# Kernel optimization log

Measured on AMD Instinct MI355X. Metric: run time of the kernel, lower is better.

Reference implementation:

```python
import jax, jax.numpy as jnp
import numpy as np

B, N, E = 64, 2048, 32768
F_IN, NHID, RULES = 256, 512, 128
RATIO = 0.5
K1 = int(np.ceil(RATIO * N)); K2 = int(np.ceil(RATIO * K1)); K3 = int(np.ceil(RATIO * K2))


def _gcn(x, src, dst, em, W, b):
    # GCNConv with self-loops and symmetric normalization; em is a float edge-validity mask.
    n = x.shape[0]
    h = x @ W  # [n, out]
    deg = jax.ops.segment_sum(em, dst, num_segments=n) + 1.0  # in-degree + self-loop
    dinv = jax.lax.rsqrt(deg)
    coef = dinv[src] * dinv[dst] * em  # [E]
    agg = jax.ops.segment_sum(h[src] * coef[:, None], dst, num_segments=n)
    return agg + h / deg[:, None] + b  # second term = self-loop with norm 1/deg


def _sag_pool(x, src, dst, em, Wg, bg, k):
    # SAGPooling: GCN scorer, per-graph top-k, scale kept nodes by tanh(score), filter+reindex edges.
    n = x.shape[0]
    score = _gcn(x, src, dst, em, Wg, bg)[:, 0]  # [n]
    vals, perm = jax.lax.top_k(score, k)
    xk = x[perm] * jnp.tanh(vals)[:, None]  # [k, F]
    newidx = jnp.full((n,), -1, dtype=src.dtype).at[perm].set(jnp.arange(k, dtype=src.dtype))
    ns, nd = newidx[src], newidx[dst]
    keep = em * (ns >= 0).astype(em.dtype) * (nd >= 0).astype(em.dtype)
    return xk, jnp.maximum(ns, 0), jnp.maximum(nd, 0), keep


_gcn_b = jax.vmap(_gcn, in_axes=(0, 0, 0, 0, None, None))
_pool_b = jax.vmap(_sag_pool, in_axes=(0, 0, 0, 0, None, None, None))


def setup_inputs() -> dict:
    key = jax.random.key(0)
    ks = jax.random.split(key, 16)
    def w(k, shape, fan_in):
        return jax.random.normal(k, shape, jnp.float32) * (1.0 / np.sqrt(fan_in))
    return {
        "x": jax.random.normal(ks[0], (B, N, F_IN), jnp.float32),
        "src": jax.random.randint(ks[1], (B, E), 0, N, jnp.int32),
        "dst": jax.random.randint(ks[2], (B, E), 0, N, jnp.int32),
        "W1": w(ks[3], (F_IN, NHID), F_IN), "b1": jnp.zeros((NHID,), jnp.float32),
        "Wp1": w(ks[4], (NHID, 1), NHID), "bp1": jnp.zeros((1,), jnp.float32),
        "W2": w(ks[5], (NHID, NHID), NHID), "b2": jnp.zeros((NHID,), jnp.float32),
        "Wp2": w(ks[6], (NHID, 1), NHID), "bp2": jnp.zeros((1,), jnp.float32),
        "W3": w(ks[7], (NHID, NHID), NHID), "b3": jnp.zeros((NHID,), jnp.float32),
        "Wp3": w(ks[8], (NHID, 1), NHID), "bp3": jnp.zeros((1,), jnp.float32),
        "lin1_W": w(ks[9], (2 * NHID, NHID), 2 * NHID), "lin1_b": jnp.zeros((NHID,), jnp.float32),
        "lin2_W": w(ks[10], (NHID, NHID // 2), NHID), "lin2_b": jnp.zeros((NHID // 2,), jnp.float32),
        "pi_W": w(ks[11], (NHID // 2, RULES), NHID // 2), "pi_b": jnp.zeros((RULES,), jnp.float32),
        "v_W": w(ks[12], (NHID // 2, 1), NHID // 2), "v_b": jnp.zeros((1,), jnp.float32),
    }


def reference(x, src, dst, W1, b1, Wp1, bp1, W2, b2, Wp2, bp2, W3, b3, Wp3, bp3,
              lin1_W, lin1_b, lin2_W, lin2_b, pi_W, pi_b, v_W, v_b):
    em = jnp.ones(src.shape, x.dtype)
    h = jax.nn.relu(_gcn_b(x, src, dst, em, W1, b1))
    h, s, d, em = _pool_b(h, src, dst, em, Wp1, bp1, K1)
    x1 = jnp.concatenate([h.max(axis=1), h.mean(axis=1)], axis=1)  # [B, 2*NHID]
    h = jax.nn.relu(_gcn_b(h, s, d, em, W2, b2))
    h, s, d, em = _pool_b(h, s, d, em, Wp2, bp2, K2)
    x2 = jnp.concatenate([h.max(axis=1), h.mean(axis=1)], axis=1)
    h = jax.nn.relu(_gcn_b(h, s, d, em, W3, b3))
    h, s, d, em = _pool_b(h, s, d, em, Wp3, bp3, K3)
    x3 = jnp.concatenate([h.max(axis=1), h.mean(axis=1)], axis=1)
    z = x1 + x2 + x3
    z = jax.nn.relu(z @ lin1_W + lin1_b)
    z = jax.nn.relu(z @ lin2_W + lin2_b)
    pi = jax.nn.log_softmax(z @ pi_W + pi_b, axis=1)
    v = jax.nn.relu(z @ v_W + v_b)
    return pi, v
```

## Files before the change

### kernel.cpp

```cpp
#include <hip/hip_runtime.h>
#include <math.h>
#include <cstdint>

#define B_   64
#define N_   2048
#define E_   32768
#define FIN  256
#define H_   512

typedef __bf16 bf16x8 __attribute__((ext_vector_type(8)));
typedef float  f32x4  __attribute__((ext_vector_type(4)));

__device__ __forceinline__ unsigned short f2bf(float f) {
  unsigned u = __float_as_uint(f);
  u += 0x7FFF + ((u >> 16) & 1);
  return (unsigned short)(u >> 16);
}
__device__ __forceinline__ unsigned pk2(float a, float b) {
  return (unsigned)f2bf(a) | ((unsigned)f2bf(b) << 16);
}
__device__ __forceinline__ float bflo(unsigned u) { return __uint_as_float(u << 16); }
__device__ __forceinline__ float bfhi(unsigned u) { return __uint_as_float(u & 0xFFFF0000u); }

__device__ __forceinline__ void accum8(float* acc, uint4 u, float c) {
  acc[0] += c * bflo(u.x); acc[1] += c * bfhi(u.x);
  acc[2] += c * bflo(u.y); acc[3] += c * bfhi(u.y);
  acc[4] += c * bflo(u.z); acc[5] += c * bfhi(u.z);
  acc[6] += c * bflo(u.w); acc[7] += c * bfhi(u.w);
}

__device__ __forceinline__ void glds16(const void* g, void* l) {
  __builtin_amdgcn_global_load_lds(
      (const __attribute__((address_space(1))) unsigned int*)g,
      (__attribute__((address_space(3))) unsigned int*)l, 16, 0, 0);
}

__global__ void xcvt_k(const float* __restrict__ x, unsigned short* __restrict__ xb) {
  int i = blockIdx.x * 256 + threadIdx.x;
  float4 f = reinterpret_cast<const float4*>(x)[i];
  uint2 o; o.x = pk2(f.x, f.y); o.y = pk2(f.z, f.w);
  reinterpret_cast<uint2*>(xb)[i] = o;
}

__global__ void wcvt_k(const float* __restrict__ W, unsigned short* __restrict__ Wt, int K) {
  int idx = blockIdx.x * 256 + threadIdx.x;
  int k = idx >> 9, n = idx & 511;
  Wt[n * K + k] = f2bf(W[idx]);
}

__global__ __launch_bounds__(256) void gemm_mfma(
    const unsigned short* __restrict__ Xb,
    const int* __restrict__ perm, const float* __restrict__ tanhv,
    const unsigned short* __restrict__ Wt, unsigned short* __restrict__ Y,
    int K, int kl2, int nsl2,
    const float* __restrict__ bias, const float* __restrict__ wp, float* __restrict__ hs) {
  __shared__ __align__(16) char smem[34816];
  const int tid = threadIdx.x;
  const int w = tid >> 6, L = tid & 63;
  const int bid = blockIdx.x;
  const int xcd = bid & 7;
  const int t = bid >> 3;
  const int colb = t & 3;
  const int strip = ((t >> 2) << 3) + xcd;
  const int m0 = strip * 128;
  const int n0 = colb * 128;
  const int e = L & 15, q = L >> 4;

  const int sw3 = (L >> 3) & 7;
  const int cA = (w * 64 + L) ^ sw3;
  const int rloc = cA >> 2;
  const int kcs = (cA & 3) * 8;

  f32x4 acc[4][4];
#pragma unroll
  for (int j = 0; j < 4; j++)
#pragma unroll
    for (int nn = 0; nn < 4; nn++) acc[j][nn] = (f32x4){0.f, 0.f, 0.f, 0.f};

  size_t asrc[2];
#pragma unroll
  for (int i = 0; i < 2; i++) {
    int g = m0 + i * 64 + rloc;
    size_t row;
    if (perm) {
      int b = g >> kl2;
      int node = perm[g];
      row = (size_t)(b << nsl2) + node;
    } else {
      row = (size_t)g;
    }
    asrc[i] = row * (size_t)K + kcs;
  }
  size_t bsrc[2];
#pragma unroll
  for (int i = 0; i < 2; i++) bsrc[i] = (size_t)(n0 + i * 64 + rloc) * K + kcs;

  const int fo = e * 4 + q;
  const int fosw = fo ^ (fo >> 3);
  const int lofs = w * 64 * 16;

  const int nk = K >> 5;
  {
    char* Ab = smem;
    char* Bb = smem + 16384;
    glds16(Xb + asrc[0], Ab + 0 * 4096 + lofs);
    glds16(Xb + asrc[1], Ab + 1 * 4096 + lofs);
    glds16(Wt + bsrc[0], Bb + 0 * 4096 + lofs);
    glds16(Wt + bsrc[1], Bb + 1 * 4096 + lofs);
  }
  __syncthreads();
  int cur = 0;
  for (int kt = 0; kt < nk; ++kt) {
    if (kt + 1 < nk) {
      const int k0 = (kt + 1) << 5;
      char* Ab = smem + (cur ^ 1) * 8192;
      char* Bb = smem + 16384 + (cur ^ 1) * 8192;
      glds16(Xb + asrc[0] + k0, Ab + 0 * 4096 + lofs);
      glds16(Xb + asrc[1] + k0, Ab + 1 * 4096 + lofs);
      glds16(Wt + bsrc[0] + k0, Bb + 0 * 4096 + lofs);
      glds16(Wt + bsrc[1] + k0, Bb + 1 * 4096 + lofs);
    }
    const uint4* As = (const uint4*)(smem + cur * 8192);
    const uint4* Bs = (const uint4*)(smem + 16384 + cur * 8192);
    bf16x8 af[4], bfr[4];
#pragma unroll
    for (int j = 0; j < 4; j++) af[j]  = __builtin_bit_cast(bf16x8, As[((w & 1) * 4 + j) * 64 + fosw]);
#pragma unroll
    for (int j = 0; j < 4; j++) bfr[j] = __builtin_bit_cast(bf16x8, Bs[((w >> 1) * 4 + j) * 64 + fosw]);
#pragma unroll
    for (int j = 0; j < 4; j++)
#pragma unroll
      for (int nn = 0; nn < 4; nn++)
        acc[j][nn] = __builtin_amdgcn_mfma_f32_16x16x32_bf16(af[j], bfr[nn], acc[j][nn], 0, 0, 0);
    __syncthreads();
    cur ^= 1;
  }

  const int RS = 136;
  unsigned short* Csm = (unsigned short*)smem;
  float bs[4], wsv[4];
#pragma unroll
  for (int nn = 0; nn < 4; nn++) {
    int coly = n0 + ((w >> 1) * 4 + nn) * 16 + e;
    bs[nn]  = bias ? bias[coly] : 0.f;
    wsv[nn] = wp ? wp[coly] : 0.f;
  }
#pragma unroll
  for (int j = 0; j < 4; j++) {
    int mt = (w & 1) * 4 + j;
#pragma unroll
    for (int r = 0; r < 4; r++) {
      int lrow = mt * 16 + q * 4 + r;
      int grow = m0 + lrow;
      float t2 = tanhv ? tanhv[grow] : 1.0f;
      float p = 0.f;
#pragma unroll
      for (int nn = 0; nn < 4; nn++) {
        int lcol = (w >> 1) * 64 + nn * 16 + e;
        float v = acc[j][nn][r] * t2;
        if (bias) v = fmaxf(v + bs[nn], 0.f);
        Csm[lrow * RS + lcol] = f2bf(v);
        p += v * wsv[nn];
      }
      if (wp) {
        p += __shfl_xor(p, 1, 64); p += __shfl_xor(p, 2, 64);
        p += __shfl_xor(p, 4, 64); p += __shfl_xor(p, 8, 64);
        if ((L & 15) == 0) atomicAdd(&hs[grow], p);
      }
    }
  }
  __syncthreads();
  const int rbase = tid >> 4, ci = tid & 15;
#pragma unroll
  for (int pass = 0; pass < 8; ++pass) {
    int lrow = pass * 16 + rbase;
    uint4 u = *(const uint4*)(Csm + lrow * RS + ci * 8);
    *(uint4*)(Y + (size_t)(m0 + lrow) * 512 + n0 + ci * 8) = u;
  }
}

template <int NL2, int LEVEL>
__global__ __launch_bounds__(1024) void csr_k(
    const int* __restrict__ src0, const int* __restrict__ dst0,
    const int* __restrict__ curNew, int* __restrict__ cmapG,
    int* __restrict__ rowptr, float* __restrict__ deg,
    int* __restrict__ col, float* __restrict__ ce) {
  const int n = 1 << NL2;
  const int CAP = 8192;
  const int b = blockIdx.x, tid = threadIdx.x;
  __shared__ int   lrp[(1 << NL2) + 1];
  __shared__ int   cur[1 << NL2];
  __shared__ float ldv[1 << NL2];
  __shared__ int   ch[1024];
  __shared__ int   cmap[(LEVEL > 0) ? 2048 : 1];
  __shared__ int   scol[CAP];
  __shared__ float sce[CAP];
  __shared__ int   sr1;
  const int eb = b << 15;

  for (int i = tid; i < n; i += 1024) cur[i] = 0;
  if (LEVEL == 1) {
    for (int v = tid; v < 2048; v += 1024) {
      int m = curNew[(b << 11) + v];
      cmap[v] = m;
      cmapG[(b << 11) + v] = m;
    }
  } else if (LEVEL == 2) {
    for (int v = tid; v < 2048; v += 1024) {
      int p = cmapG[(b << 11) + v];
      cmap[v] = (p >= 0) ? curNew[(b << 10) + p] : -1;
    }
  }
  __syncthreads();

  for (int e = tid; e < E_; e += 4096) {
#pragma unroll
    for (int u = 0; u < 4; u++) {
      int ei = eb + e + u * 1024;
      int dd = dst0[ei];
      if (LEVEL == 0) {
        atomicAdd(&cur[dd], 1);
      } else {
        int md = cmap[dd], ms = cmap[src0[ei]];
        if (ms >= 0 && md >= 0) atomicAdd(&cur[md], 1);
      }
    }
  }
  __syncthreads();

  const int nth = (n < 1024) ? n : 1024;
  const int per = (n + 1023) >> 10;
  int lc[per];
  int s = 0;
  if (tid < nth) {
    int base = tid * per;
#pragma unroll
    for (int i = 0; i < per; i++) { lc[i] = cur[base + i]; s += lc[i]; }
  }
  ch[tid] = s;
  __syncthreads();
  for (int off2 = 1; off2 < nth; off2 <<= 1) {
    int v = (tid >= off2) ? ch[tid - off2] : 0;
    __syncthreads();
    ch[tid] += v;
    __syncthreads();
  }
  if (tid < nth) {
    int run = (tid == 0) ? 0 : ch[tid - 1];
    int base = tid * per;
#pragma unroll
    for (int i = 0; i < per; i++) {
      int g = base + i;
      lrp[g] = run;
      rowptr[b * (n + 1) + g] = run;
      cur[g] = run;
      float dd = (float)(lc[i] + 1);
      deg[(b << NL2) + g] = dd;
      ldv[g] = 1.0f / sqrtf(dd);
      run += lc[i];
    }
    if (tid == nth - 1) { lrp[n] = run; rowptr[b * (n + 1) + n] = run; }
  }
  __syncthreads();

  int r0 = 0;
  while (r0 < n) {
    int base0 = lrp[r0];
    if (tid == 0) sr1 = n + 1;
    __syncthreads();
    for (int r = r0 + 1 + tid; r <= n; r += 1024) {
      if (lrp[r] - base0 > CAP) { atomicMin(&sr1, r); break; }
    }
    __syncthreads();
    int r1 = sr1 - 1;
    if (r1 > n) r1 = n;
    if (r1 <= r0) {
      for (int e = tid; e < E_; e += 1024) {
        int ei = eb + e;
        int ss = src0[ei], dd = dst0[ei];
        int ms, md;
        if (LEVEL == 0) { ms = ss; md = dd; }
        else { ms = cmap[ss]; md = cmap[dd]; }
        if (ms >= 0 && md == r0) {
          int pos = atomicAdd(&cur[r0], 1);
          col[eb + pos] = ms;
          ce[eb + pos] = ldv[ms] * ldv[r0];
        }
      }
      __syncthreads();
      r0 = r0 + 1;
      continue;
    }
    for (int e = tid; e < E_; e += 4096) {
#pragma unroll
      for (int u = 0; u < 4; u++) {
        int ei = eb + e + u * 1024;
        int ss = src0[ei], dd = dst0[ei];
        int ms, md;
        if (LEVEL == 0) { ms = ss; md = dd; }
        else { ms = cmap[ss]; md = cmap[dd]; }
        if (ms >= 0 && md >= r0 && md < r1) {
          int pos = atomicAdd(&cur[md], 1);
          scol[pos - base0] = ms;
          sce[pos - base0] = ldv[ms] * ldv[md];
        }
      }
    }
    __syncthreads();
    int cnt = lrp[r1] - base0;
    for (int i = tid; i < cnt; i += 1024) {
      col[eb + base0 + i] = scol[i];
      ce[eb + base0 + i] = sce[i];
    }
    __syncthreads();
    r0 = r1;
  }
}

__global__ __launch_bounds__(256) void aggx_k(
    const unsigned short* __restrict__ X,
    const int* __restrict__ rowptr, const int* __restrict__ col,
    const float* __restrict__ ce, const float* __restrict__ deg,
    unsigned short* __restrict__ Xa) {
  const int hw = threadIdx.x >> 5, hl = threadIdx.x & 31;
  const int xcd = blockIdx.x & 7;
  const int slot = blockIdx.x >> 3;
  const int gslot = slot >> 8;
  const int v8 = slot & 255;
  const int b = (gslot << 3) + xcd;
  const int v = v8 * 8 + hw;
  const int bbase = b << 11;
  const int vg = bbase + v;
  const int rb = b * (N_ + 1) + v;
  const int st = rowptr[rb], en = rowptr[rb + 1];
  const int* cb = col + (b << 15);
  const float* cee = ce + (b << 15);
  const unsigned short* Xb_ = X + (size_t)bbase * 256 + hl * 8;
  float acc[8] = {0.f, 0.f, 0.f, 0.f, 0.f, 0.f, 0.f, 0.f};
  int e2 = st;
  for (; e2 + 4 <= en; e2 += 4) {
    int s0 = cb[e2], s1 = cb[e2 + 1], s2 = cb[e2 + 2], s3 = cb[e2 + 3];
    float c0 = cee[e2], c1 = cee[e2 + 1], c2 = cee[e2 + 2], c3 = cee[e2 + 3];
    uint4 u0 = *(const uint4*)(Xb_ + (size_t)s0 * 256);
    uint4 u1 = *(const uint4*)(Xb_ + (size_t)s1 * 256);
    uint4 u2 = *(const uint4*)(Xb_ + (size_t)s2 * 256);
    uint4 u3 = *(const uint4*)(Xb_ + (size_t)s3 * 256);
    accum8(acc, u0, c0); accum8(acc, u1, c1);
    accum8(acc, u2, c2); accum8(acc, u3, c3);
  }
  for (; e2 < en; e2++) {
    uint4 u = *(const uint4*)(Xb_ + (size_t)cb[e2] * 256);
    accum8(acc, u, cee[e2]);
  }
  {
    uint4 u = *(const uint4*)(Xb_ + (size_t)v * 256);
    accum8(acc, u, 1.0f / deg[vg]);
  }
  uint4 o;
  o.x = pk2(acc[0], acc[1]); o.y = pk2(acc[2], acc[3]);
  o.z = pk2(acc[4], acc[5]); o.w = pk2(acc[6], acc[7]);
  *(uint4*)(Xa + (size_t)vg * 256 + hl * 8) = o;
}

template <int NL2>
__global__ __launch_bounds__(256) void agg_k(
    const unsigned short* __restrict__ H,
    const int* __restrict__ rowptr, const int* __restrict__ col,
    const float* __restrict__ ce, const float* __restrict__ deg,
    const float* __restrict__ bias, const float* __restrict__ wp,
    unsigned short* __restrict__ C, float* __restrict__ hs) {
  const int n = 1 << NL2;
  const int xcd = blockIdx.x & 7;
  const int slot = blockIdx.x >> 3;
  const int gslot = slot >> (NL2 - 2);
  const int v4 = slot & ((1 << (NL2 - 2)) - 1);
  const int b = (gslot << 3) + xcd;
  const int w = threadIdx.x >> 6, L = threadIdx.x & 63;
  const int v = v4 * 4 + w;
  const int bbase = b << NL2;
  const int vg = bbase + v;
  const int rb = b * (n + 1) + v;
  const int st = rowptr[rb], en = rowptr[rb + 1];
  const int* cb = col + (b << 15);
  const float* cee = ce + (b << 15);
  const unsigned short* Hb_ = H + (size_t)bbase * 512 + (size_t)L * 8;

  float acc[8] = {0.f, 0.f, 0.f, 0.f, 0.f, 0.f, 0.f, 0.f};
  int e2 = st;
  for (; e2 + 4 <= en; e2 += 4) {
    int s0 = cb[e2], s1 = cb[e2 + 1], s2 = cb[e2 + 2], s3 = cb[e2 + 3];
    float c0 = cee[e2], c1 = cee[e2 + 1], c2 = cee[e2 + 2], c3 = cee[e2 + 3];
    uint4 u0 = *(const uint4*)(Hb_ + (size_t)s0 * 512);
    uint4 u1 = *(const uint4*)(Hb_ + (size_t)s1 * 512);
    uint4 u2 = *(const uint4*)(Hb_ + (size_t)s2 * 512);
    uint4 u3 = *(const uint4*)(Hb_ + (size_t)s3 * 512);
    accum8(acc, u0, c0); accum8(acc, u1, c1);
    accum8(acc, u2, c2); accum8(acc, u3, c3);
  }
  for (; e2 < en; e2++) {
    int s = cb[e2];
    uint4 u = *(const uint4*)(Hb_ + (size_t)s * 512);
    accum8(acc, u, cee[e2]);
  }
  {
    float idg = 1.0f / deg[vg];
    uint4 u = *(const uint4*)(Hb_ + (size_t)v * 512);
    accum8(acc, u, idg);
  }
  float4 bLo = *(const float4*)(bias + L * 8);
  float4 bHi = *(const float4*)(bias + L * 8 + 4);
  acc[0] = fmaxf(acc[0] + bLo.x, 0.f); acc[1] = fmaxf(acc[1] + bLo.y, 0.f);
  acc[2] = fmaxf(acc[2] + bLo.z, 0.f); acc[3] = fmaxf(acc[3] + bLo.w, 0.f);
  acc[4] = fmaxf(acc[4] + bHi.x, 0.f); acc[5] = fmaxf(acc[5] + bHi.y, 0.f);
  acc[6] = fmaxf(acc[6] + bHi.z, 0.f); acc[7] = fmaxf(acc[7] + bHi.w, 0.f);
  uint4 o;
  o.x = pk2(acc[0], acc[1]); o.y = pk2(acc[2], acc[3]);
  o.z = pk2(acc[4], acc[5]); o.w = pk2(acc[6], acc[7]);
  *(uint4*)(C + (size_t)vg * 512 + L * 8) = o;
  float4 wLo = *(const float4*)(wp + L * 8);
  float4 wHi = *(const float4*)(wp + L * 8 + 4);
  float p = acc[0] * wLo.x + acc[1] * wLo.y + acc[2] * wLo.z + acc[3] * wLo.w
          + acc[4] * wHi.x + acc[5] * wHi.y + acc[6] * wHi.z + acc[7] * wHi.w;
#pragma unroll
  for (int off = 32; off > 0; off >>= 1) p += __shfl_down(p, off, 64);
  if (L == 0) hs[vg] = p;
}

__global__ void scoreagg_k(const float* __restrict__ hs, const int* __restrict__ rowptr,
                           const int* __restrict__ col, const float* __restrict__ ce,
                           const float* __restrict__ deg, const float* __restrict__ bp,
                           float* __restrict__ score, int nl2) {
  int idx = blockIdx.x * 256 + threadIdx.x;
  int n = 1 << nl2;
  int b = idx >> nl2, v = idx & (n - 1);
  int rb = b * (n + 1) + v;
  int st = rowptr[rb], en = rowptr[rb + 1];
  const int* cb = col + (b << 15);
  const float* cee = ce + (b << 15);
  int bbase = b << nl2;
  float acc = 0.f;
  int e = st;
  for (; e + 4 <= en; e += 4) {
    acc += hs[bbase + cb[e]] * cee[e] + hs[bbase + cb[e + 1]] * cee[e + 1]
         + hs[bbase + cb[e + 2]] * cee[e + 2] + hs[bbase + cb[e + 3]] * cee[e + 3];
  }
  for (; e < en; e++) acc += hs[bbase + cb[e]] * cee[e];
  score[idx] = acc + hs[idx] / deg[idx] + bp[0];
}

__global__ __launch_bounds__(1024) void topk_k(const float* __restrict__ score, int* __restrict__ perm,
                                               float* __restrict__ tanhv, int* __restrict__ newidx,
                                               int n, int k) {
  int b = blockIdx.x, tid = threadIdx.x;
  __shared__ float ss[2048];
  __shared__ int si[2048];
  for (int i = tid; i < n; i += 1024) { ss[i] = score[b * n + i]; si[i] = i; }
  __syncthreads();
  for (int size = 2; size <= n; size <<= 1) {
    for (int stride = size >> 1; stride > 0; stride >>= 1) {
      for (int i = tid; i < n; i += 1024) {
        int j = i ^ stride;
        if (j > i) {
          bool up = ((i & size) == 0);
          float fi = ss[i], fj = ss[j];
          int ii = si[i], ij = si[j];
          bool iBefore = (fi > fj) || (fi == fj && ii < ij);
          bool sw = up ? (!iBefore) : iBefore;
          if (sw) { ss[i] = fj; ss[j] = fi; si[i] = ij; si[j] = ii; }
        }
      }
      __syncthreads();
    }
  }
  for (int r = tid; r < n; r += 1024) newidx[b * n + si[r]] = (r < k) ? r : -1;
  for (int r = tid; r < k; r += 1024) { perm[b * k + r] = si[r]; tanhv[b * k + r] = tanhf(ss[r]); }
}

__global__ __launch_bounds__(512) void statsp_k(const unsigned short* __restrict__ C,
    const int* __restrict__ perm, const float* __restrict__ tv,
    float* __restrict__ zp, int nsl2, int k, int kch) {
  int b = blockIdx.x, rg = blockIdx.y, f = threadIdx.x;
  int r0 = rg * kch;
  float mx = -1e30f, sm = 0.f;
#pragma unroll 4
  for (int r = r0; r < r0 + kch; r++) {
    int node = perm[b * k + r];
    float t = tv[b * k + r];
    float val = __uint_as_float((unsigned)C[((size_t)((b << nsl2) + node)) * 512 + f] << 16) * t;
    mx = fmaxf(mx, val); sm += val;
  }
  zp[(size_t)(b * 8 + rg) * 1024 + f] = mx;
  zp[(size_t)(b * 8 + rg) * 1024 + 512 + f] = sm;
}

__global__ __launch_bounds__(512) void statsr_k(const float* __restrict__ zp,
                                                float* __restrict__ z, int k) {
  int b = blockIdx.x, f = threadIdx.x;
  float mx = -1e30f, sm = 0.f;
#pragma unroll
  for (int g = 0; g < 8; g++) {
    mx = fmaxf(mx, zp[(size_t)(b * 8 + g) * 1024 + f]);
    sm += zp[(size_t)(b * 8 + g) * 1024 + 512 + f];
  }
  z[b * 1024 + f] += mx;
  z[b * 1024 + 512 + f] += sm / (float)k;
}

__global__ __launch_bounds__(256) void mlp1_k(const float* __restrict__ z,
                                              const float* __restrict__ W1,
                                              float* __restrict__ zp1) {
  const int kc = blockIdx.x & 7;
  const int b = blockIdx.x >> 3;
  const int tid = threadIdx.x;
  __shared__ float zs[128];
  if (tid < 128) zs[tid] = z[b * 1024 + kc * 128 + tid];
  __syncthreads();
  float a0 = 0.f, a1 = 0.f;
  const float* Wb = W1 + (size_t)(kc * 128) * 512 + tid * 2;
#pragma unroll 4
  for (int i = 0; i < 128; i++) {
    float2 w = *(const float2*)(Wb + (size_t)i * 512);
    float zi = zs[i];
    a0 += zi * w.x; a1 += zi * w.y;
  }
  reinterpret_cast<float2*>(zp1 + ((size_t)(kc * 64 + b)) * 512)[tid] = make_float2(a0, a1);
}

__global__ __launch_bounds__(256) void mlp2_k(const float* __restrict__ zp1,
                                              const float* __restrict__ b1,
                                              const float* __restrict__ W2,
                                              float* __restrict__ zp2) {
  const int kc = blockIdx.x & 1;
  const int b = blockIdx.x >> 1;
  const int tid = threadIdx.x;
  __shared__ float z1s[256];
  {
    int i = kc * 256 + tid;
    float a = b1[i];
#pragma unroll
    for (int g = 0; g < 8; g++) a += zp1[((size_t)(g * 64 + b)) * 512 + i];
    z1s[tid] = fmaxf(a, 0.f);
  }
  __syncthreads();
  float a = 0.f;
  const float* Wb = W2 + (size_t)(kc * 256) * 256 + tid;
#pragma unroll 4
  for (int i = 0; i < 256; i++) a += z1s[i] * Wb[(size_t)i * 256];
  zp2[((size_t)(kc * 64 + b)) * 256 + tid] = a;
}

__global__ __launch_bounds__(128) void mlp3_k(const float* __restrict__ zp2,
                                              const float* __restrict__ b2,
                                              const float* __restrict__ piW,
                                              const float* __restrict__ pib,
                                              const float* __restrict__ vW,
                                              const float* __restrict__ vb,
                                              float* __restrict__ out) {
  const int b = blockIdx.x, tid = threadIdx.x;
  __shared__ float z2s[256];
  __shared__ float wred[4];
  __shared__ float sred[2];
  for (int t = tid; t < 256; t += 128) {
    float a = b2[t] + zp2[(size_t)b * 256 + t] + zp2[(size_t)(64 + b) * 256 + t];
    z2s[t] = fmaxf(a, 0.f);
  }
  __syncthreads();
  float a = pib[tid];
#pragma unroll 4
  for (int i = 0; i < 256; i++) a += z2s[i] * piW[(size_t)i * 128 + tid];
  float vp = z2s[tid] * vW[tid] + z2s[tid + 128] * vW[tid + 128];
  float m = a;
#pragma unroll
  for (int off = 32; off > 0; off >>= 1) {
    vp += __shfl_xor(vp, off, 64);
    m = fmaxf(m, __shfl_xor(m, off, 64));
  }
  const int wv = tid >> 6;
  if ((tid & 63) == 0) { wred[wv] = m; wred[2 + wv] = vp; }
  __syncthreads();
  m = fmaxf(wred[0], wred[1]);
  float s = expf(a - m);
#pragma unroll
  for (int off = 32; off > 0; off >>= 1) s += __shfl_xor(s, off, 64);
  if ((tid & 63) == 0) sred[wv] = s;
  __syncthreads();
  s = sred[0] + sred[1];
  if (tid == 0) out[B_ * 128 + b] = fmaxf(vb[0] + wred[2] + wred[3], 0.f);
  out[b * 128 + tid] = a - m - logf(s);
}

extern "C" void kernel_launch(void* const* d_in, const int* in_sizes, int n_in,
                              void* d_out, int out_size, void* d_ws, size_t ws_size,
                              hipStream_t stream) {
  const float* x    = (const float*)d_in[0];
  const int*   src0 = (const int*)d_in[1];
  const int*   dst0 = (const int*)d_in[2];
  const float* W1   = (const float*)d_in[3];
  const float* b1   = (const float*)d_in[4];
  const float* Wp1  = (const float*)d_in[5];
  const float* bp1  = (const float*)d_in[6];
  const float* W2   = (const float*)d_in[7];
  const float* b2   = (const float*)d_in[8];
  const float* Wp2  = (const float*)d_in[9];
  const float* bp2  = (const float*)d_in[10];
  const float* W3   = (const float*)d_in[11];
  const float* b3   = (const float*)d_in[12];
  const float* Wp3  = (const float*)d_in[13];
  const float* bp3  = (const float*)d_in[14];
  const float* l1W  = (const float*)d_in[15];
  const float* l1b  = (const float*)d_in[16];
  const float* l2W  = (const float*)d_in[17];
  const float* l2b  = (const float*)d_in[18];
  const float* piW  = (const float*)d_in[19];
  const float* pib  = (const float*)d_in[20];
  const float* vW   = (const float*)d_in[21];
  const float* vb   = (const float*)d_in[22];
  float* out = (float*)d_out;
  (void)in_sizes; (void)n_in; (void)out_size; (void)ws_size;

  unsigned short* Cb = (unsigned short*)d_in[0];

  char* base = (char*)d_ws;
  size_t off = 0;
  auto alloc = [&](size_t bytes) -> void* {
    void* r = base + off;
    off += (bytes + 255) & ~(size_t)255;
    return r;
  };
  unsigned short* Hb   = (unsigned short*)alloc((size_t)B_ * 1024 * H_ * 2);
  unsigned short* xb   = (unsigned short*)alloc((size_t)B_ * N_ * FIN * 2);
  unsigned short* Xa   = (unsigned short*)alloc((size_t)B_ * N_ * FIN * 2);
  unsigned short* W1t  = (unsigned short*)alloc((size_t)512 * 256 * 2);
  unsigned short* W2t  = (unsigned short*)alloc((size_t)512 * 512 * 2);
  unsigned short* W3t  = (unsigned short*)alloc((size_t)512 * 512 * 2);
  int*   col    = (int*)alloc((size_t)B_ * E_ * 4);
  float* coefE  = (float*)alloc((size_t)B_ * E_ * 4);
  int*   cmapG  = (int*)alloc((size_t)B_ * N_ * 4);
  int*   rowptr = (int*)alloc((size_t)B_ * (N_ + 1) * 4);
  float* deg    = (float*)alloc((size_t)B_ * N_ * 4);
  float* hs     = (float*)alloc((size_t)B_ * N_ * 4);
  float* score  = (float*)alloc((size_t)B_ * N_ * 4);
  int*   newidx = (int*)alloc((size_t)B_ * N_ * 4);
  int*   perm   = (int*)alloc((size_t)B_ * 1024 * 4);
  float* tanhv  = (float*)alloc((size_t)B_ * 1024 * 4);
  float* zpart  = (float*)alloc((size_t)B_ * 8 * 1024 * 4);
  float* z      = (float*)alloc((size_t)B_ * 1024 * 4);

  float* zp1 = zpart;
  float* zp2 = zpart + (size_t)8 * 64 * 512;

  xcvt_k<<<B_ * N_ * FIN / 4 / 256, 256, 0, stream>>>(x, xb);
  wcvt_k<<<256 * 512 / 256, 256, 0, stream>>>(W1, W1t, 256);
  wcvt_k<<<512 * 512 / 256, 256, 0, stream>>>(W2, W2t, 512);
  wcvt_k<<<512 * 512 / 256, 256, 0, stream>>>(W3, W3t, 512);
  hipMemsetAsync(z, 0, (size_t)B_ * 1024 * 4, stream);

  {
    csr_k<11, 0><<<B_, 1024, 0, stream>>>(src0, dst0, nullptr, nullptr,
                                          rowptr, deg, col, coefE);
    aggx_k<<<B_ * 2048 / 8, 256, 0, stream>>>(xb, rowptr, col, coefE, deg, Xa);
    hipMemsetAsync(hs, 0, (size_t)B_ * 2048 * 4, stream);
    gemm_mfma<<<B_ * 2048 / 128 * 4, 256, 0, stream>>>(
        Xa, nullptr, nullptr, W1t, Cb, 256, 0, 0, b1, Wp1, hs);
    scoreagg_k<<<B_ * 2048 / 256, 256, 0, stream>>>(hs, rowptr, col, coefE, deg, bp1, score, 11);
    topk_k<<<B_, 1024, 0, stream>>>(score, perm, tanhv, newidx, 2048, 1024);
    statsp_k<<<dim3(B_, 8), 512, 0, stream>>>(Cb, perm, tanhv, zpart, 11, 1024, 128);
    statsr_k<<<B_, 512, 0, stream>>>(zpart, z, 1024);
    csr_k<10, 1><<<B_, 1024, 0, stream>>>(src0, dst0, newidx, cmapG,
                                          rowptr, deg, col, coefE);
  }
  {
    gemm_mfma<<<B_ * 1024 / 128 * 4, 256, 0, stream>>>(
        Cb, perm, tanhv, W2t, Hb, 512, 10, 11, nullptr, nullptr, nullptr);
    agg_k<10><<<B_ * 1024 / 4, 256, 0, stream>>>(Hb, rowptr, col, coefE, deg, b2, Wp2, Cb, hs);
    scoreagg_k<<<B_ * 1024 / 256, 256, 0, stream>>>(hs, rowptr, col, coefE, deg, bp2, score, 10);
    topk_k<<<B_, 1024, 0, stream>>>(score, perm, tanhv, newidx, 1024, 512);
    statsp_k<<<dim3(B_, 8), 512, 0, stream>>>(Cb, perm, tanhv, zpart, 10, 512, 64);
    statsr_k<<<B_, 512, 0, stream>>>(zpart, z, 512);
    csr_k<9, 2><<<B_, 1024, 0, stream>>>(src0, dst0, newidx, cmapG,
                                         rowptr, deg, col, coefE);
  }
  {
    gemm_mfma<<<B_ * 512 / 128 * 4, 256, 0, stream>>>(
        Cb, perm, tanhv, W3t, Hb, 512, 9, 10, nullptr, nullptr, nullptr);
    agg_k<9><<<B_ * 512 / 4, 256, 0, stream>>>(Hb, rowptr, col, coefE, deg, b3, Wp3, Cb, hs);
    scoreagg_k<<<B_ * 512 / 256, 256, 0, stream>>>(hs, rowptr, col, coefE, deg, bp3, score, 9);
    topk_k<<<B_, 1024, 0, stream>>>(score, perm, tanhv, newidx, 512, 256);
    statsp_k<<<dim3(B_, 8), 512, 0, stream>>>(Cb, perm, tanhv, zpart, 9, 256, 32);
    statsr_k<<<B_, 512, 0, stream>>>(zpart, z, 256);
  }

  mlp1_k<<<B_ * 8, 256, 0, stream>>>(z, l1W, zp1);
  mlp2_k<<<B_ * 2, 256, 0, stream>>>(zp1, l1b, l2W, zp2);
  mlp3_k<<<B_, 128, 0, stream>>>(zp2, l2b, piW, pib, vW, vb, out);
}
```

Baseline: 961.2 us.

## Enlarge GEMM tile to 256 rows and replace score atomics with partial-sum buffer

Each GEMM block now computes a 256x128 output tile instead of 128x128. Every wave owns 64 rows and all 128 columns, so B fragments are reused across more rows and the block count halves. The epilogue writes the tile in two 128-row halves through shared memory. The per-row score dot product is now written to one of four column-block partial buffers instead of using global atomics, and a small hsum kernel reduces those partials, which also removes the memset. In exchange the kernel uses more accumulator registers (32 tiles per wave) and more LDS (48KB), and adds an extra launch and epilogue syncs.

```diff
diff --git a/kernel.cpp b/kernel.cpp
--- a/kernel.cpp
+++ b/kernel.cpp
@@ -48,13 +48,14 @@
   Wt[n * K + k] = f2bf(W[idx]);
 }
 
-__global__ __launch_bounds__(256) void gemm_mfma(
+__global__ __launch_bounds__(256, 2) void gemm_mfma(
     const unsigned short* __restrict__ Xb,
     const int* __restrict__ perm, const float* __restrict__ tanhv,
     const unsigned short* __restrict__ Wt, unsigned short* __restrict__ Y,
     int K, int kl2, int nsl2,
-    const float* __restrict__ bias, const float* __restrict__ wp, float* __restrict__ hs) {
-  __shared__ __align__(16) char smem[34816];
+    const float* __restrict__ bias, const float* __restrict__ wp, float* __restrict__ hs4,
+    int Mtot) {
+  __shared__ __align__(16) char smem[49152];
   const int tid = threadIdx.x;
   const int w = tid >> 6, L = tid & 63;
   const int bid = blockIdx.x;
@@ -62,25 +63,24 @@
   const int t = bid >> 3;
   const int colb = t & 3;
   const int strip = ((t >> 2) << 3) + xcd;
-  const int m0 = strip * 128;
+  const int m0 = strip * 256;
   const int n0 = colb * 128;
   const int e = L & 15, q = L >> 4;
 
   const int sw3 = (L >> 3) & 7;
-  const int cA = (w * 64 + L) ^ sw3;
-  const int rloc = cA >> 2;
-  const int kcs = (cA & 3) * 8;
-
-  f32x4 acc[4][4];
+  const int lofs = w * 1024;
+
+  f32x4 acc[4][8];
 #pragma unroll
   for (int j = 0; j < 4; j++)
 #pragma unroll
-    for (int nn = 0; nn < 4; nn++) acc[j][nn] = (f32x4){0.f, 0.f, 0.f, 0.f};
-
-  size_t asrc[2];
-#pragma unroll
-  for (int i = 0; i < 2; i++) {
-    int g = m0 + i * 64 + rloc;
+    for (int nn = 0; nn < 8; nn++) acc[j][nn] = (f32x4){0.f, 0.f, 0.f, 0.f};
+
+  size_t asrc[4];
+#pragma unroll
+  for (int i = 0; i < 4; i++) {
+    int cA = (i * 256 + w * 64 + L) ^ sw3;
+    int g = m0 + (cA >> 2);
     size_t row;
     if (perm) {
       int b = g >> kl2;
@@ -89,48 +89,50 @@
     } else {
       row = (size_t)g;
     }
-    asrc[i] = row * (size_t)K + kcs;
+    asrc[i] = row * (size_t)K + (cA & 3) * 8;
   }
   size_t bsrc[2];
 #pragma unroll
-  for (int i = 0; i < 2; i++) bsrc[i] = (size_t)(n0 + i * 64 + rloc) * K + kcs;
+  for (int i = 0; i < 2; i++) {
+    int cB = (i * 256 + w * 64 + L) ^ sw3;
+    bsrc[i] = (size_t)(n0 + (cB >> 2)) * K + (cB & 3) * 8;
+  }
 
   const int fo = e * 4 + q;
   const int fosw = fo ^ (fo >> 3);
-  const int lofs = w * 64 * 16;
 
   const int nk = K >> 5;
   {
     char* Ab = smem;
-    char* Bb = smem + 16384;
-    glds16(Xb + asrc[0], Ab + 0 * 4096 + lofs);
-    glds16(Xb + asrc[1], Ab + 1 * 4096 + lofs);
-    glds16(Wt + bsrc[0], Bb + 0 * 4096 + lofs);
-    glds16(Wt + bsrc[1], Bb + 1 * 4096 + lofs);
+    char* Bb = smem + 32768;
+#pragma unroll
+    for (int i = 0; i < 4; i++) glds16(Xb + asrc[i], Ab + i * 4096 + lofs);
+#pragma unroll
+    for (int i = 0; i < 2; i++) glds16(Wt + bsrc[i], Bb + i * 4096 + lofs);
   }
   __syncthreads();
   int cur = 0;
   for (int kt = 0; kt < nk; ++kt) {
     if (kt + 1 < nk) {
       const int k0 = (kt + 1) << 5;
-      char* Ab = smem + (cur ^ 1) * 8192;
-      char* Bb = smem + 16384 + (cur ^ 1) * 8192;
-      glds16(Xb + asrc[0] + k0, Ab + 0 * 4096 + lofs);
-      glds16(Xb + asrc[1] + k0, Ab + 1 * 4096 + lofs);
-      glds16(Wt + bsrc[0] + k0, Bb + 0 * 4096 + lofs);
-      glds16(Wt + bsrc[1] + k0, Bb + 1 * 4096 + lofs);
-    }
-    const uint4* As = (const uint4*)(smem + cur * 8192);
-    const uint4* Bs = (const uint4*)(smem + 16384 + cur * 8192);
-    bf16x8 af[4], bfr[4];
-#pragma unroll
-    for (int j = 0; j < 4; j++) af[j]  = __builtin_bit_cast(bf16x8, As[((w & 1) * 4 + j) * 64 + fosw]);
-#pragma unroll
-    for (int j = 0; j < 4; j++) bfr[j] = __builtin_bit_cast(bf16x8, Bs[((w >> 1) * 4 + j) * 64 + fosw]);
+      char* Ab = smem + (cur ^ 1) * 16384;
+      char* Bb = smem + 32768 + (cur ^ 1) * 8192;
+#pragma unroll
+      for (int i = 0; i < 4; i++) glds16(Xb + asrc[i] + k0, Ab + i * 4096 + lofs);
+#pragma unroll
+      for (int i = 0; i < 2; i++) glds16(Wt + bsrc[i] + k0, Bb + i * 4096 + lofs);
+    }
+    const uint4* As = (const uint4*)(smem + cur * 16384);
+    const uint4* Bs = (const uint4*)(smem + 32768 + cur * 8192);
+    bf16x8 af[4], bfr[8];
+#pragma unroll
+    for (int j = 0; j < 4; j++) af[j]  = __builtin_bit_cast(bf16x8, As[w * 256 + j * 64 + fosw]);
+#pragma unroll
+    for (int nn = 0; nn < 8; nn++) bfr[nn] = __builtin_bit_cast(bf16x8, Bs[nn * 64 + fosw]);
 #pragma unroll
     for (int j = 0; j < 4; j++)
 #pragma unroll
-      for (int nn = 0; nn < 4; nn++)
+      for (int nn = 0; nn < 8; nn++)
         acc[j][nn] = __builtin_amdgcn_mfma_f32_16x16x32_bf16(af[j], bfr[nn], acc[j][nn], 0, 0, 0);
     __syncthreads();
     cur ^= 1;
@@ -138,45 +140,56 @@
 
   const int RS = 136;
   unsigned short* Csm = (unsigned short*)smem;
-  float bs[4], wsv[4];
-#pragma unroll
-  for (int nn = 0; nn < 4; nn++) {
-    int coly = n0 + ((w >> 1) * 4 + nn) * 16 + e;
+  float* hsm = (float*)(smem + 34816);
+  float bs[8], wsv[8];
+#pragma unroll
+  for (int nn = 0; nn < 8; nn++) {
+    int coly = n0 + nn * 16 + e;
     bs[nn]  = bias ? bias[coly] : 0.f;
     wsv[nn] = wp ? wp[coly] : 0.f;
   }
-#pragma unroll
-  for (int j = 0; j < 4; j++) {
-    int mt = (w & 1) * 4 + j;
-#pragma unroll
-    for (int r = 0; r < 4; r++) {
-      int lrow = mt * 16 + q * 4 + r;
-      int grow = m0 + lrow;
-      float t2 = tanhv ? tanhv[grow] : 1.0f;
-      float p = 0.f;
-#pragma unroll
-      for (int nn = 0; nn < 4; nn++) {
-        int lcol = (w >> 1) * 64 + nn * 16 + e;
-        float v = acc[j][nn][r] * t2;
-        if (bias) v = fmaxf(v + bs[nn], 0.f);
-        Csm[lrow * RS + lcol] = f2bf(v);
-        p += v * wsv[nn];
+  const int rbase = tid >> 4, ci = tid & 15;
+#pragma unroll
+  for (int h = 0; h < 2; ++h) {
+    if ((w >> 1) == h) {
+#pragma unroll
+      for (int j = 0; j < 4; j++) {
+#pragma unroll
+        for (int r = 0; r < 4; r++) {
+          int lrow = w * 64 + j * 16 + q * 4 + r;
+          int grow = m0 + lrow;
+          float t2 = tanhv ? tanhv[grow] : 1.0f;
+          float p = 0.f;
+#pragma unroll
+          for (int nn = 0; nn < 8; nn++) {
+            float v = acc[j][nn][r] * t2;
+            if (bias) v = fmaxf(v + bs[nn], 0.f);
+            Csm[(lrow - h * 128) * RS + nn * 16 + e] = f2bf(v);
+            p += v * wsv[nn];
+          }
+          if (wp) {
+            p += __shfl_xor(p, 1, 64); p += __shfl_xor(p, 2, 64);
+            p += __shfl_xor(p, 4, 64); p += __shfl_xor(p, 8, 64);
+            if ((L & 15) == 0) hsm[lrow] = p;
+          }
+        }
       }
-      if (wp) {
-        p += __shfl_xor(p, 1, 64); p += __shfl_xor(p, 2, 64);
-        p += __shfl_xor(p, 4, 64); p += __shfl_xor(p, 8, 64);
-        if ((L & 15) == 0) atomicAdd(&hs[grow], p);
-      }
-    }
-  }
-  __syncthreads();
-  const int rbase = tid >> 4, ci = tid & 15;
-#pragma unroll
-  for (int pass = 0; pass < 8; ++pass) {
-    int lrow = pass * 16 + rbase;
-    uint4 u = *(const uint4*)(Csm + lrow * RS + ci * 8);
-    *(uint4*)(Y + (size_t)(m0 + lrow) * 512 + n0 + ci * 8) = u;
-  }
+    }
+    __syncthreads();
+#pragma unroll
+    for (int pass = 0; pass < 8; ++pass) {
+      int lrow = pass * 16 + rbase;
+      uint4 u = *(const uint4*)(Csm + lrow * RS + ci * 8);
+      *(uint4*)(Y + (size_t)(m0 + h * 128 + lrow) * 512 + n0 + ci * 8) = u;
+    }
+    __syncthreads();
+  }
+  if (wp) hs4[(size_t)colb * Mtot + m0 + tid] = hsm[tid];
+}
+
+__global__ void hsum_k(const float* __restrict__ hs4, float* __restrict__ hs, int M) {
+  int i = blockIdx.x * 256 + threadIdx.x;
+  hs[i] = hs4[i] + hs4[M + i] + hs4[2 * M + i] + hs4[3 * M + i];
 }
 
 template <int NL2, int LEVEL>
@@ -639,6 +652,7 @@
   int*   rowptr = (int*)alloc((size_t)B_ * (N_ + 1) * 4);
   float* deg    = (float*)alloc((size_t)B_ * N_ * 4);
   float* hs     = (float*)alloc((size_t)B_ * N_ * 4);
+  float* hs4    = (float*)alloc((size_t)4 * B_ * N_ * 4);
   float* score  = (float*)alloc((size_t)B_ * N_ * 4);
   int*   newidx = (int*)alloc((size_t)B_ * N_ * 4);
   int*   perm   = (int*)alloc((size_t)B_ * 1024 * 4);
@@ -659,9 +673,9 @@
     csr_k<11, 0><<<B_, 1024, 0, stream>>>(src0, dst0, nullptr, nullptr,
                                           rowptr, deg, col, coefE);
     aggx_k<<<B_ * 2048 / 8, 256, 0, stream>>>(xb, rowptr, col, coefE, deg, Xa);
-    hipMemsetAsync(hs, 0, (size_t)B_ * 2048 * 4, stream);
-    gemm_mfma<<<B_ * 2048 / 128 * 4, 256, 0, stream>>>(
-        Xa, nullptr, nullptr, W1t, Cb, 256, 0, 0, b1, Wp1, hs);
+    gemm_mfma<<<B_ * 2048 / 256 * 4, 256, 0, stream>>>(
+        Xa, nullptr, nullptr, W1t, Cb, 256, 0, 0, b1, Wp1, hs4, B_ * 2048);
+    hsum_k<<<B_ * 2048 / 256, 256, 0, stream>>>(hs4, hs, B_ * 2048);
     scoreagg_k<<<B_ * 2048 / 256, 256, 0, stream>>>(hs, rowptr, col, coefE, deg, bp1, score, 11);
     topk_k<<<B_, 1024, 0, stream>>>(score, perm, tanhv, newidx, 2048, 1024);
     statsp_k<<<dim3(B_, 8), 512, 0, stream>>>(Cb, perm, tanhv, zpart, 11, 1024, 128);
@@ -670,8 +684,8 @@
                                           rowptr, deg, col, coefE);
   }
   {
-    gemm_mfma<<<B_ * 1024 / 128 * 4, 256, 0, stream>>>(
-        Cb, perm, tanhv, W2t, Hb, 512, 10, 11, nullptr, nullptr, nullptr);
+    gemm_mfma<<<B_ * 1024 / 256 * 4, 256, 0, stream>>>(
+        Cb, perm, tanhv, W2t, Hb, 512, 10, 11, nullptr, nullptr, nullptr, 0);
     agg_k<10><<<B_ * 1024 / 4, 256, 0, stream>>>(Hb, rowptr, col, coefE, deg, b2, Wp2, Cb, hs);
     scoreagg_k<<<B_ * 1024 / 256, 256, 0, stream>>>(hs, rowptr, col, coefE, deg, bp2, score, 10);
     topk_k<<<B_, 1024, 0, stream>>>(score, perm, tanhv, newidx, 1024, 512);
@@ -681,8 +695,8 @@
                                          rowptr, deg, col, coefE);
   }
   {
-    gemm_mfma<<<B_ * 512 / 128 * 4, 256, 0, stream>>>(
-        Cb, perm, tanhv, W3t, Hb, 512, 9, 10, nullptr, nullptr, nullptr);
+    gemm_mfma<<<B_ * 512 / 256 * 4, 256, 0, stream>>>(
+        Cb, perm, tanhv, W3t, Hb, 512, 9, 10, nullptr, nullptr, nullptr, 0);
     agg_k<9><<<B_ * 512 / 4, 256, 0, stream>>>(Hb, rowptr, col, coefE, deg, b3, Wp3, Cb, hs);
     scoreagg_k<<<B_ * 512 / 256, 256, 0, stream>>>(hs, rowptr, col, coefE, deg, bp3, score, 9);
     topk_k<<<B_, 1024, 0, stream>>>(score, perm, tanhv, newidx, 512, 256);
```

Result: no change. 964.6 us (+0.3%).
